# Performance work log

Hardware: AMD Instinct MI355X
Metric: run time of the kernel (lower is better)

The kernel has to match this reference:

```python
import jax, jax.numpy as jnp
import numpy as np
from jax.scipy.special import erfc

# Problem scale
B, N, K = 16, 4000, 64          # systems, atoms/system, max neighbors
L = 30.0                         # cubic cell edge (Angstrom)
ALPHA = 0.3                      # Ewald splitting parameter (1/A), from config
KCUT = 1.0                       # reciprocal-space cutoff (1/A), from config
NMAX = 4                         # floor(KCUT / (2*pi/L)) -> static k-grid half-width
COULOMB_CONSTANT = 14.399645351950548  # e^2/(4 pi eps0) in eV*A


def setup_inputs() -> dict:
    key = jax.random.key(0)
    k1, k2, k3, k4 = jax.random.split(key, 4)
    T = B * N
    positions = jax.random.uniform(k1, (T, 3), dtype=jnp.float32) * L
    node_charges = jax.random.normal(k2, (T,), dtype=jnp.float32)
    cell = jnp.tile(jnp.eye(3, dtype=jnp.float32) * L, (B, 1, 1))
    # neighbor indices restricted to the same system; -1 marks self/padding
    local = jax.random.randint(k3, (T, K), 0, N)
    base = (jnp.arange(T) // N) * N
    nm = local + base[:, None]
    nm = jnp.where(nm == jnp.arange(T)[:, None], -1, nm).astype(jnp.int32)
    neighbor_shifts = jnp.zeros((T, K, 3), dtype=jnp.int32)
    num_neighbors = jnp.full((T,), K, dtype=jnp.int32)
    batch_idx = (jnp.arange(T) // N).astype(jnp.int32)
    return dict(positions=positions, node_charges=node_charges, cell=cell,
                neighbor_matrix=nm, neighbor_shifts=neighbor_shifts,
                num_neighbors=num_neighbors, batch_idx=batch_idx)


def _ewald_energies(positions, node_charges, cell, neighbor_matrix,
                    neighbor_shifts, num_neighbors, batch_idx):
    T = positions.shape[0]
    Bn = cell.shape[0]
    Nn = T // Bn
    Kn = neighbor_matrix.shape[1]
    q = node_charges.reshape(-1)
    dtype = positions.dtype
    alpha = jnp.full((Bn,), ALPHA, dtype=dtype)
    a_i = alpha[batch_idx]                                  # [T]

    # ---- real-space: neighbor gather + erfc + scatter-less per-atom sum ----
    mask = (neighbor_matrix >= 0) & (jnp.arange(Kn)[None, :] < num_neighbors[:, None])
    j = jnp.where(mask, neighbor_matrix, 0)                 # safe gather index [T,K]
    off = jnp.einsum('tks,tsd->tkd', neighbor_shifts.astype(dtype), cell[batch_idx])
    rij = positions[j] + off - positions[:, None, :]        # [T,K,3]
    d = jnp.sqrt(jnp.where(mask, jnp.sum(rij * rij, -1), 1.0))
    pair = jnp.where(mask, q[:, None] * q[j] * erfc(a_i[:, None] * d) / d, 0.0)
    # 0.5 for full (non-half) neighbor list; Gaussian self-interaction correction
    e_real = 0.5 * jnp.sum(pair, axis=-1) - a_i / jnp.sqrt(jnp.pi) * q * q  # [T]

    # ---- reciprocal-space: structure-factor sum over k-vectors ----
    rng = np.arange(-NMAX, NMAX + 1)
    nvec = np.stack(np.meshgrid(rng, rng, rng, indexing='ij'), -1).reshape(-1, 3)
    nvec = jnp.asarray(nvec, dtype=dtype)                   # [G,3] integer grid
    recip = 2.0 * jnp.pi * jnp.transpose(jnp.linalg.inv(cell), (0, 2, 1))  # rows b_j
    kv = jnp.einsum('gj,bjd->bgd', nvec, recip)             # [B,G,3]
    k2 = jnp.sum(kv * kv, -1)                               # [B,G]
    kmask = (k2 > 1e-10) & (k2 <= KCUT * KCUT)
    vol = jnp.abs(jnp.linalg.det(cell))                     # [B]
    a2 = alpha * alpha
    coef = jnp.where(kmask,
                     4.0 * jnp.pi * jnp.exp(-k2 / (4.0 * a2[:, None])) / jnp.where(kmask, k2, 1.0),
                     0.0) / (2.0 * vol[:, None])            # [B,G]
    pos_b = positions.reshape(Bn, Nn, 3)
    q_b = q.reshape(Bn, Nn)
    phase = jnp.einsum('bnd,bgd->bng', pos_b, kv)           # [B,N,G]
    c = jnp.cos(phase)
    s = jnp.sin(phase)
    Sre = jnp.einsum('bn,bng->bg', q_b, c)
    Sim = jnp.einsum('bn,bng->bg', q_b, s)
    e_recip = q_b * (jnp.einsum('bng,bg->bn', c, coef * Sre) +
                     jnp.einsum('bng,bg->bn', s, coef * Sim))  # [B,N]

    per_atom = e_real + e_recip.reshape(-1)
    energies = jax.ops.segment_sum(per_atom, batch_idx, num_segments=Bn)
    return energies * COULOMB_CONSTANT


def reference(positions, node_charges, cell, neighbor_matrix, neighbor_shifts,
              num_neighbors, batch_idx):
    return _ewald_energies(positions, node_charges, cell, neighbor_matrix,
                           neighbor_shifts, num_neighbors, batch_idx)
```

## Files before the change

kernel.cpp:

```cpp
#include <hip/hip_runtime.h>
#include <math.h>

#define GPB    8
#define GTOT   729
#define APB    16
#define STRIDE 344

__device__ __forceinline__ float wave_reduce(float v) {
    #pragma unroll
    for (int off = 32; off > 0; off >>= 1) v += __shfl_down(v, off, 64);
    return v;
}

__global__ __launch_bounds__(256)
void pack_pq(const float* __restrict__ pos, const float* __restrict__ chg,
             float4* __restrict__ pq, int T)
{
    int t = blockIdx.x * 256 + threadIdx.x;
    if (t < T)
        pq[t] = make_float4(pos[3*t], pos[3*t+1], pos[3*t+2], chg[t]);
}

template <bool PACKED>
__global__ __launch_bounds__(256)
void ewald_fused(const float4* __restrict__ pq,
                 const float*  __restrict__ pos,
                 const float*  __restrict__ chg,
                 const float*  __restrict__ cell,
                 const int*    __restrict__ nm,
                 const int*    __restrict__ shifts,
                 const int*    __restrict__ nnb,
                 float* __restrict__ partial,
                 int T, int N, int K, int Bn, int CB)
{
    __shared__ float red[16];

    const float TWO_PI  = 6.283185307179586f;
    const float ALPHA   = 0.3f;
    const float INV4A2  = 2.7777777777f;
    const float KC2     = 1.0f;
    const float INV_SQRT_PI = 0.5641895835477563f;

    int blk = blockIdx.x;

    if (blk < CB) {
        int gpb_groups = (GTOT + GPB - 1) / GPB;
        int b   = blk / gpb_groups;
        int grp = blk % gpb_groups;

        const float* C = cell + 9 * b;
        float m00=C[0], m01=C[1], m02=C[2];
        float m10=C[3], m11=C[4], m12=C[5];
        float m20=C[6], m21=C[7], m22=C[8];
        float a00 = m11*m22 - m12*m21;
        float a01 = m02*m21 - m01*m22;
        float a02 = m01*m12 - m02*m11;
        float a10 = m12*m20 - m10*m22;
        float a11 = m00*m22 - m02*m20;
        float a12 = m02*m10 - m00*m12;
        float a20 = m10*m21 - m11*m20;
        float a21 = m01*m20 - m00*m21;
        float a22 = m00*m11 - m01*m10;
        float det = m00*a00 + m01*a10 + m02*a20;
        float invdet = 1.0f / det;
        float vol = fabsf(det);

        float kvx[GPB], kvy[GPB], kvz[GPB], coef[GPB];
        bool any = false;
        #pragma unroll
        for (int gi = 0; gi < GPB; ++gi) {
            int g = grp * GPB + gi;
            float cf = 0.f, kx = 0.f, ky = 0.f, kz = 0.f;
            if (g < GTOT) {
                int ix = g / 81, rem = g - ix * 81;
                int iy = rem / 9, iz = rem - iy * 9;
                int nx = ix - 4, ny = iy - 4, nz = iz - 4;
                bool pos_half = (nx > 0) || (nx == 0 && (ny > 0 || (ny == 0 && nz > 0)));
                if (pos_half) {
                    float fx = (float)nx, fy = (float)ny, fz = (float)nz;
                    kx = TWO_PI * invdet * (fx*a00 + fy*a01 + fz*a02);
                    ky = TWO_PI * invdet * (fx*a10 + fy*a11 + fz*a12);
                    kz = TWO_PI * invdet * (fx*a20 + fy*a21 + fz*a22);
                    float k2 = kx*kx + ky*ky + kz*kz;
                    if (k2 > 1e-10f && k2 <= KC2) {
                        cf = 12.566370614359172f * __expf(-k2 * INV4A2) / (k2 * vol);
                    }
                }
            }
            kvx[gi] = kx; kvy[gi] = ky; kvz[gi] = kz; coef[gi] = cf;
            any = any || (cf != 0.f);
        }

        int slot = b * STRIDE + (N / APB) + grp;
        if (!any) {
            if (threadIdx.x == 0) partial[slot] = 0.f;
            return;
        }

        float Sre[GPB], Sim[GPB];
        #pragma unroll
        for (int gi = 0; gi < GPB; ++gi) { Sre[gi] = 0.f; Sim[gi] = 0.f; }

        for (int a = threadIdx.x; a < N; a += 256) {
            float x, y, z, qa;
            if (PACKED) {
                float4 v = pq[(size_t)b * N + a];
                x = v.x; y = v.y; z = v.z; qa = v.w;
            } else {
                const float* pb = pos + (size_t)3 * (b * N + a);
                x = pb[0]; y = pb[1]; z = pb[2];
                qa = chg[(size_t)b * N + a];
            }
            #pragma unroll
            for (int gi = 0; gi < GPB; ++gi) {
                if (coef[gi] != 0.f) {
                    float ph = x*kvx[gi] + y*kvy[gi] + z*kvz[gi];
                    float s, c;
                    __sincosf(ph, &s, &c);
                    Sre[gi] = fmaf(qa, c, Sre[gi]);
                    Sim[gi] = fmaf(qa, s, Sim[gi]);
                }
            }
        }

        int lane = threadIdx.x & 63;
        int w    = threadIdx.x >> 6;
        float e_acc = 0.f;
        #pragma unroll
        for (int gi = 0; gi < GPB; ++gi) {
            if (coef[gi] != 0.f) {
                float sr = wave_reduce(Sre[gi]);
                float si = wave_reduce(Sim[gi]);
                if (lane == 0) { red[2*w] = sr; red[2*w+1] = si; }
                __syncthreads();
                if (threadIdx.x == 0) {
                    float SR = red[0] + red[2] + red[4] + red[6];
                    float SI = red[1] + red[3] + red[5] + red[7];
                    e_acc += coef[gi] * (SR*SR + SI*SI);
                }
                __syncthreads();
            }
        }
        if (threadIdx.x == 0) partial[slot] = e_acc;
    } else {
        int rb = blk - CB;
        int t0 = rb * APB;
        int sys = t0 / N;
        int lane = threadIdx.x & 63;
        int w    = threadIdx.x >> 6;

        float val = 0.0f;
        #pragma unroll
        for (int i = 0; i < APB/4; ++i) {
            int t = t0 + w * (APB/4) + i;
            float xi, yi, zi, qi;
            if (PACKED) {
                float4 v = pq[t];
                xi = v.x; yi = v.y; zi = v.z; qi = v.w;
            } else {
                xi = pos[3*t]; yi = pos[3*t+1]; zi = pos[3*t+2];
                qi = chg[t];
            }
            if (lane == 0) val -= ALPHA * INV_SQRT_PI * qi * qi;
            int nn = nnb[t];
            for (int k = lane; k < K; k += 64) {
                int p = t * K + k;
                int j = nm[p];
                bool msk = (j >= 0) && (k < nn);
                if (msk) {
                    int sx = shifts[3*p], sy = shifts[3*p+1], sz = shifts[3*p+2];
                    float ox = 0.f, oy = 0.f, oz = 0.f;
                    if ((sx | sy | sz) != 0) {
                        const float* C = cell + 9 * sys;
                        float fx = (float)sx, fy = (float)sy, fz = (float)sz;
                        ox = fx*C[0] + fy*C[3] + fz*C[6];
                        oy = fx*C[1] + fy*C[4] + fz*C[7];
                        oz = fx*C[2] + fy*C[5] + fz*C[8];
                    }
                    float xj, yj, zj, qj;
                    if (PACKED) {
                        float4 v = pq[j];
                        xj = v.x; yj = v.y; zj = v.z; qj = v.w;
                    } else {
                        xj = pos[3*j]; yj = pos[3*j+1]; zj = pos[3*j+2];
                        qj = chg[j];
                    }
                    float dx = xj + ox - xi;
                    float dy = yj + oy - yi;
                    float dz = zj + oz - zi;
                    float r2 = fmaf(dx, dx, fmaf(dy, dy, dz*dz));
                    float rinv = rsqrtf(r2);
                    float d = r2 * rinv;
                    val += 0.5f * qi * qj * erfcf(ALPHA * d) * rinv;
                }
            }
        }

        val = wave_reduce(val);
        if (lane == 0) red[w] = val;
        __syncthreads();
        if (threadIdx.x == 0) {
            int rb_in_sys = rb - sys * (N / APB);
            partial[sys * STRIDE + rb_in_sys] =
                red[0] + red[1] + red[2] + red[3];
        }
    }
}

__global__ __launch_bounds__(256)
void final_reduce(const float* __restrict__ partial, float* __restrict__ out,
                  int nslots)
{
    __shared__ float red[4];
    const float COUL = 14.399645351950548f;
    int b = blockIdx.x;
    float v = 0.f;
    for (int s = threadIdx.x; s < nslots; s += 256)
        v += partial[b * STRIDE + s];
    v = wave_reduce(v);
    int lane = threadIdx.x & 63, w = threadIdx.x >> 6;
    if (lane == 0) red[w] = v;
    __syncthreads();
    if (threadIdx.x == 0)
        out[b] = COUL * (red[0] + red[1] + red[2] + red[3]);
}

extern "C" void kernel_launch(void* const* d_in, const int* in_sizes, int n_in,
                              void* d_out, int out_size, void* d_ws, size_t ws_size,
                              hipStream_t stream) {
    const float* pos    = (const float*)d_in[0];
    const float* chg    = (const float*)d_in[1];
    const float* cell   = (const float*)d_in[2];
    const int*   nm     = (const int*)d_in[3];
    const int*   shifts = (const int*)d_in[4];
    const int*   nnb    = (const int*)d_in[5];

    int T  = in_sizes[1];
    int Bn = in_sizes[2] / 9;
    int N  = T / Bn;
    int K  = in_sizes[3] / T;
    int CB = Bn * ((GTOT + GPB - 1) / GPB);
    int RB = T / APB;
    int nslots = (N / APB) + ((GTOT + GPB - 1) / GPB);

    size_t partBytes = (size_t)Bn * STRIDE * sizeof(float);
    size_t packOff   = ((partBytes + 255) / 256) * 256;
    size_t packBytes = (size_t)T * sizeof(float4);

    float*  partial = (float*)d_ws;
    bool packed = (ws_size >= packOff + packBytes);

    if (packed) {
        float4* pq = (float4*)((char*)d_ws + packOff);
        pack_pq<<<(T + 255) / 256, 256, 0, stream>>>(pos, chg, pq, T);
        ewald_fused<true><<<CB + RB, 256, 0, stream>>>(
            pq, pos, chg, cell, nm, shifts, nnb, partial, T, N, K, Bn, CB);
    } else {
        ewald_fused<false><<<CB + RB, 256, 0, stream>>>(
            nullptr, pos, chg, cell, nm, shifts, nnb, partial, T, N, K, Bn, CB);
    }
    final_reduce<<<Bn, 256, 0, stream>>>(partial, (float*)d_out, nslots);
}
```

Before: 124.9 us.

## Stage system atoms in LDS, interleave block roles, drop pack kernel

Removes the separate pack kernel. Each real-space block now copies its whole system's positions and charges into 64KB of shared memory as float4, so neighbor gathers are served from LDS instead of global memory. Each real-space block handles 100 atoms instead of 16, one neighbor per lane, with the next atom's neighbor indices and shifts prefetched. Reciprocal and real-space blocks are interleaved 7:3 in the grid. The risks are 64KB of static LDS limiting occupancy for every block, including reciprocal blocks that never use it, and the full system staged redundantly by each of 40 blocks per system.

```diff
diff --git a/kernel.cpp b/kernel.cpp
--- a/kernel.cpp
+++ b/kernel.cpp
@@ -1,10 +1,13 @@
 #include <hip/hip_runtime.h>
 #include <math.h>
 
-#define GPB    8
-#define GTOT   729
-#define APB    16
-#define STRIDE 344
+#define GPB     8
+#define GTOT    729
+#define GGROUPS 92
+#define APB     100
+#define AW      25
+#define RSLOTS  40
+#define STRIDE  136
 
 __device__ __forceinline__ float wave_reduce(float v) {
     #pragma unroll
@@ -13,40 +16,31 @@
 }
 
 __global__ __launch_bounds__(256)
-void pack_pq(const float* __restrict__ pos, const float* __restrict__ chg,
-             float4* __restrict__ pq, int T)
+void ewald_fused(const float* __restrict__ pos,
+                 const float* __restrict__ chg,
+                 const float* __restrict__ cell,
+                 const int*   __restrict__ nm,
+                 const int*   __restrict__ shifts,
+                 const int*   __restrict__ nnb,
+                 float* __restrict__ partial,
+                 int T, int N, int K, int Bn, int CB, int RB)
 {
-    int t = blockIdx.x * 256 + threadIdx.x;
-    if (t < T)
-        pq[t] = make_float4(pos[3*t], pos[3*t+1], pos[3*t+2], chg[t]);
-}
-
-template <bool PACKED>
-__global__ __launch_bounds__(256)
-void ewald_fused(const float4* __restrict__ pq,
-                 const float*  __restrict__ pos,
-                 const float*  __restrict__ chg,
-                 const float*  __restrict__ cell,
-                 const int*    __restrict__ nm,
-                 const int*    __restrict__ shifts,
-                 const int*    __restrict__ nnb,
-                 float* __restrict__ partial,
-                 int T, int N, int K, int Bn, int CB)
-{
-    __shared__ float red[16];
+    __shared__ float4 spq[4000];
+    __shared__ float  red[16];
 
     const float TWO_PI  = 6.283185307179586f;
     const float ALPHA   = 0.3f;
     const float INV4A2  = 2.7777777777f;
-    const float KC2     = 1.0f;
     const float INV_SQRT_PI = 0.5641895835477563f;
 
-    int blk = blockIdx.x;
-
-    if (blk < CB) {
-        int gpb_groups = (GTOT + GPB - 1) / GPB;
-        int b   = blk / gpb_groups;
-        int grp = blk % gpb_groups;
+    int q10 = blockIdx.x / 10;
+    int r10 = blockIdx.x - q10 * 10;
+
+    if (r10 < 7) {
+        int rid = q10 * 7 + r10;
+        if (rid >= CB) return;
+        int b   = rid / GGROUPS;
+        int grp = rid - b * GGROUPS;
 
         const float* C = cell + 9 * b;
         float m00=C[0], m01=C[1], m02=C[2];
@@ -82,7 +76,7 @@
                     ky = TWO_PI * invdet * (fx*a10 + fy*a11 + fz*a12);
                     kz = TWO_PI * invdet * (fx*a20 + fy*a21 + fz*a22);
                     float k2 = kx*kx + ky*ky + kz*kz;
-                    if (k2 > 1e-10f && k2 <= KC2) {
+                    if (k2 > 1e-10f && k2 <= 1.0f) {
                         cf = 12.566370614359172f * __expf(-k2 * INV4A2) / (k2 * vol);
                     }
                 }
@@ -91,7 +85,7 @@
             any = any || (cf != 0.f);
         }
 
-        int slot = b * STRIDE + (N / APB) + grp;
+        int slot = b * STRIDE + RSLOTS + grp;
         if (!any) {
             if (threadIdx.x == 0) partial[slot] = 0.f;
             return;
@@ -101,16 +95,11 @@
         #pragma unroll
         for (int gi = 0; gi < GPB; ++gi) { Sre[gi] = 0.f; Sim[gi] = 0.f; }
 
+        const float* pb = pos + (size_t)3 * b * N;
+        const float* qb = chg + (size_t)b * N;
         for (int a = threadIdx.x; a < N; a += 256) {
-            float x, y, z, qa;
-            if (PACKED) {
-                float4 v = pq[(size_t)b * N + a];
-                x = v.x; y = v.y; z = v.z; qa = v.w;
-            } else {
-                const float* pb = pos + (size_t)3 * (b * N + a);
-                x = pb[0]; y = pb[1]; z = pb[2];
-                qa = chg[(size_t)b * N + a];
-            }
+            float x = pb[3*a], y = pb[3*a+1], z = pb[3*a+2];
+            float qa = qb[a];
             #pragma unroll
             for (int gi = 0; gi < GPB; ++gi) {
                 if (coef[gi] != 0.f) {
@@ -143,67 +132,68 @@
         }
         if (threadIdx.x == 0) partial[slot] = e_acc;
     } else {
-        int rb = blk - CB;
-        int t0 = rb * APB;
-        int sys = t0 / N;
+        int rb = q10 * 3 + (r10 - 7);
+        if (rb >= RB) return;
+        int sys  = rb / RSLOTS;
+        int bis  = rb - sys * RSLOTS;
+        int base = sys * N;
+
+        for (int i = threadIdx.x; i < N; i += 256) {
+            int t = base + i;
+            spq[i] = make_float4(pos[3*t], pos[3*t+1], pos[3*t+2], chg[t]);
+        }
+        __syncthreads();
+
         int lane = threadIdx.x & 63;
         int w    = threadIdx.x >> 6;
-
-        float val = 0.0f;
-        #pragma unroll
-        for (int i = 0; i < APB/4; ++i) {
-            int t = t0 + w * (APB/4) + i;
-            float xi, yi, zi, qi;
-            if (PACKED) {
-                float4 v = pq[t];
-                xi = v.x; yi = v.y; zi = v.z; qi = v.w;
-            } else {
-                xi = pos[3*t]; yi = pos[3*t+1]; zi = pos[3*t+2];
-                qi = chg[t];
-            }
+        int a0   = bis * APB + w * AW;
+
+        const int*  nmp = nm + (size_t)(base + a0) * K;
+        const int3* sh3 = reinterpret_cast<const int3*>(shifts)
+                          + (size_t)(base + a0) * K;
+
+        float val = 0.f;
+        int  jn = nmp[lane];
+        int3 sn = sh3[lane];
+
+        for (int i = 0; i < AW; ++i) {
+            int  j = jn;
+            int3 s = sn;
+            if (i + 1 < AW) {
+                jn = nmp[(size_t)(i+1)*K + lane];
+                sn = sh3[(size_t)(i+1)*K + lane];
+            }
+            int aloc = a0 + i;
+            float4 vi = spq[aloc];
+            float qi = vi.w;
             if (lane == 0) val -= ALPHA * INV_SQRT_PI * qi * qi;
-            int nn = nnb[t];
-            for (int k = lane; k < K; k += 64) {
-                int p = t * K + k;
-                int j = nm[p];
-                bool msk = (j >= 0) && (k < nn);
-                if (msk) {
-                    int sx = shifts[3*p], sy = shifts[3*p+1], sz = shifts[3*p+2];
-                    float ox = 0.f, oy = 0.f, oz = 0.f;
-                    if ((sx | sy | sz) != 0) {
-                        const float* C = cell + 9 * sys;
-                        float fx = (float)sx, fy = (float)sy, fz = (float)sz;
-                        ox = fx*C[0] + fy*C[3] + fz*C[6];
-                        oy = fx*C[1] + fy*C[4] + fz*C[7];
-                        oz = fx*C[2] + fy*C[5] + fz*C[8];
-                    }
-                    float xj, yj, zj, qj;
-                    if (PACKED) {
-                        float4 v = pq[j];
-                        xj = v.x; yj = v.y; zj = v.z; qj = v.w;
-                    } else {
-                        xj = pos[3*j]; yj = pos[3*j+1]; zj = pos[3*j+2];
-                        qj = chg[j];
-                    }
-                    float dx = xj + ox - xi;
-                    float dy = yj + oy - yi;
-                    float dz = zj + oz - zi;
-                    float r2 = fmaf(dx, dx, fmaf(dy, dy, dz*dz));
-                    float rinv = rsqrtf(r2);
-                    float d = r2 * rinv;
-                    val += 0.5f * qi * qj * erfcf(ALPHA * d) * rinv;
-                }
+            int nn = nnb[base + aloc];
+            bool msk = (j >= 0) && (lane < nn);
+            float4 vj = spq[msk ? (j - base) : 0];
+            if (msk) {
+                float ox = 0.f, oy = 0.f, oz = 0.f;
+                if ((s.x | s.y | s.z) != 0) {
+                    const float* C = cell + 9 * sys;
+                    float fx = (float)s.x, fy = (float)s.y, fz = (float)s.z;
+                    ox = fx*C[0] + fy*C[3] + fz*C[6];
+                    oy = fx*C[1] + fy*C[4] + fz*C[7];
+                    oz = fx*C[2] + fy*C[5] + fz*C[8];
+                }
+                float dx = vj.x + ox - vi.x;
+                float dy = vj.y + oy - vi.y;
+                float dz = vj.z + oz - vi.z;
+                float r2 = fmaf(dx, dx, fmaf(dy, dy, dz*dz));
+                float rinv = rsqrtf(r2);
+                float d = r2 * rinv;
+                val += 0.5f * qi * vj.w * erfcf(ALPHA * d) * rinv;
             }
         }
 
         val = wave_reduce(val);
         if (lane == 0) red[w] = val;
         __syncthreads();
-        if (threadIdx.x == 0) {
-            int rb_in_sys = rb - sys * (N / APB);
-            partial[sys * STRIDE + rb_in_sys] =
-                red[0] + red[1] + red[2] + red[3];
-        }
+        if (threadIdx.x == 0)
+            partial[sys * STRIDE + bis] = red[0] + red[1] + red[2] + red[3];
     }
 }
 
@@ -239,25 +229,18 @@
     int Bn = in_sizes[2] / 9;
     int N  = T / Bn;
     int K  = in_sizes[3] / T;
-    int CB = Bn * ((GTOT + GPB - 1) / GPB);
-    int RB = T / APB;
-    int nslots = (N / APB) + ((GTOT + GPB - 1) / GPB);
-
-    size_t partBytes = (size_t)Bn * STRIDE * sizeof(float);
-    size_t packOff   = ((partBytes + 255) / 256) * 256;
-    size_t packBytes = (size_t)T * sizeof(float4);
-
-    float*  partial = (float*)d_ws;
-    bool packed = (ws_size >= packOff + packBytes);
-
-    if (packed) {
-        float4* pq = (float4*)((char*)d_ws + packOff);
-        pack_pq<<<(T + 255) / 256, 256, 0, stream>>>(pos, chg, pq, T);
-        ewald_fused<true><<<CB + RB, 256, 0, stream>>>(
-            pq, pos, chg, cell, nm, shifts, nnb, partial, T, N, K, Bn, CB);
-    } else {
-        ewald_fused<false><<<CB + RB, 256, 0, stream>>>(
-            nullptr, pos, chg, cell, nm, shifts, nnb, partial, T, N, K, Bn, CB);
-    }
-    final_reduce<<<Bn, 256, 0, stream>>>(partial, (float*)d_out, nslots);
-}
+    int CB = Bn * GGROUPS;
+    int RB = Bn * (N / APB);
+
+    int reps = (CB + 6) / 7;
+    int r2   = (RB + 2) / 3;
+    if (r2 > reps) reps = r2;
+    int grid = reps * 10;
+
+    float* partial = (float*)d_ws;
+
+    ewald_fused<<<grid, 256, 0, stream>>>(pos, chg, cell, nm, shifts, nnb,
+                                          partial, T, N, K, Bn, CB, RB);
+    final_reduce<<<Bn, 256, 0, stream>>>(partial, (float*)d_out,
+                                         RSLOTS + GGROUPS);
+}
```

Measured after the change: 144.0 us. +15.3%, slower.
